# Kernel tuning notes

Measured on AMD Instinct MI355X. Metric: run time of the kernel, lower is better.

## Reference

```python
import jax, jax.numpy as jnp
import numpy as np

B, C, N = 2, 256, 8192
CI = 256  # inter_channels
EPS = 1e-5


def setup_inputs() -> dict:
    key = jax.random.key(0)
    ks = jax.random.split(key, 11)
    s = 1.0 / np.sqrt(C)
    si = 1.0 / np.sqrt(CI)
    return {
        "x": jax.random.normal(ks[0], (B, C, N), dtype=jnp.float32),
        "g_w": jax.random.uniform(ks[1], (CI, C), jnp.float32, -s, s),
        "g_b": jax.random.uniform(ks[2], (CI,), jnp.float32, -s, s),
        "theta_w": jax.random.uniform(ks[3], (CI, C), jnp.float32, -s, s),
        "theta_b": jax.random.uniform(ks[4], (CI,), jnp.float32, -s, s),
        "phi_w": jax.random.uniform(ks[5], (CI, C), jnp.float32, -s, s),
        "phi_b": jax.random.uniform(ks[6], (CI,), jnp.float32, -s, s),
        "w_w": jax.random.uniform(ks[7], (CI, CI), jnp.float32, -si, si),
        "w_b": jax.random.uniform(ks[8], (CI,), jnp.float32, -si, si),
        "bn_gamma": jax.random.normal(ks[9], (CI,), dtype=jnp.float32),
        "bn_beta": jax.random.normal(ks[10], (CI,), dtype=jnp.float32),
    }


def reference(x, g_w, g_b, theta_w, theta_b, phi_w, phi_b, w_w, w_b, bn_gamma, bn_beta):
    # 1x1 Conv1d == channel-wise linear: (o,c) @ (b,c,n) -> (b,o,n)
    g_x = jnp.einsum('oc,bcn->bno', g_w, x) + g_b            # (b, n, ci)
    theta_x = jnp.einsum('oc,bcn->bno', theta_w, x) + theta_b  # (b, n, ci)
    phi_x = jnp.einsum('oc,bcn->bon', phi_w, x) + phi_b[:, None]  # (b, ci, n)
    f = jnp.einsum('bnc,bcm->bnm', theta_x, phi_x)           # (b, n, n), unscaled
    f_div_C = jax.nn.softmax(f, axis=-1)
    y = jnp.einsum('bnm,bmc->bcn', f_div_C, g_x)             # (b, ci, n)
    # W: 1x1 conv then BatchNorm1d (training-mode batch statistics)
    z = jnp.einsum('oc,bcn->bon', w_w, y) + w_b[:, None]     # (b, ci, n)
    mean = jnp.mean(z, axis=(0, 2), keepdims=True)
    var = jnp.mean(jnp.square(z - mean), axis=(0, 2), keepdims=True)  # biased var
    z_hat = (z - mean) * jax.lax.rsqrt(var + EPS)
    out = bn_gamma[:, None] * z_hat + bn_beta[:, None]
    return out
```

## Files before the change

kernel.cpp:

```cpp
#include <hip/hip_runtime.h>
#include <hip/hip_bf16.h>
#include <stdint.h>

#define BB  2
#define CC  256
#define NN  8192
#define CIc 256

typedef __attribute__((ext_vector_type(4)))  float f32x4;
typedef __attribute__((ext_vector_type(16))) float f32x16;
typedef __attribute__((ext_vector_type(8)))  short s16x8;
typedef __attribute__((ext_vector_type(4)))  short s16x4;
typedef __attribute__((ext_vector_type(4)))  int   i32x4;

static __device__ __forceinline__ short f2bf(float f) {
    union { float f; unsigned u; } v; v.f = f;
    unsigned r = (v.u + 0x7FFFu + ((v.u >> 16) & 1u)) >> 16;
    return (short)r;
}
static __device__ __forceinline__ float bf2f(short h) {
    union { unsigned u; float f; } v; v.u = ((unsigned)(unsigned short)h) << 16;
    return v.f;
}

static __device__ __forceinline__ void gload16(const void* g, void* l) {
    __builtin_amdgcn_global_load_lds(
        (const __attribute__((address_space(1))) unsigned int*)g,
        (__attribute__((address_space(3))) unsigned int*)l, 16, 0, 0);
}

__global__ __launch_bounds__(256) void pack_kernel(
    const float* __restrict__ tw, const float* __restrict__ pw,
    const float* __restrict__ gw, const float* __restrict__ ww,
    short* __restrict__ Wf)
{
    int gid  = blockIdx.x * 256 + threadIdx.x;
    int lane = gid & 63;
    int grp  = gid >> 6;
    int ks = grp & 7, ot = (grp >> 3) & 15, m = grp >> 7;
    const float* W = (m == 0) ? tw : (m == 1) ? pw : (m == 2) ? gw : ww;
    const float* p = &W[(size_t)(ot * 16 + (lane & 15)) * 256 + ks * 32 + (lane >> 4) * 8];
    float4 a = *(const float4*)p, c = *(const float4*)(p + 4);
    s16x8 o;
    o[0] = f2bf(a.x); o[1] = f2bf(a.y); o[2] = f2bf(a.z); o[3] = f2bf(a.w);
    o[4] = f2bf(c.x); o[5] = f2bf(c.y); o[6] = f2bf(c.z); o[7] = f2bf(c.w);
    *(s16x8*)&Wf[(size_t)gid * 8] = o;
}

__global__ __launch_bounds__(256) void proj_kernel(
    const float* __restrict__ x, const short* __restrict__ Wf,
    const float* __restrict__ tb, const float* __restrict__ pb,
    const float* __restrict__ gb,
    short* __restrict__ Qb, short* __restrict__ Kf, short* __restrict__ Vf)
{
    __shared__ char xls[64 * 512];
    const int blk = blockIdx.x;
    const int m   = blk % 3;
    const int r2  = blk / 3;
    const int b   = r2 >> 7;
    const int n0  = (r2 & 127) << 6;
    const int tid = threadIdx.x;

    for (int it = 0; it < 16; ++it) {
        int chunk = it * 256 + tid;
        int c  = chunk >> 4;
        int n4 = (chunk & 15) << 2;
        const float4 v = *(const float4*)&x[((size_t)b * CC + c) * NN + n0 + n4];
        float vv[4] = {v.x, v.y, v.z, v.w};
        #pragma unroll
        for (int j = 0; j < 4; ++j) {
            int row = n4 + j;
            int addr = row * 512 + ((c * 2) ^ ((row & 31) << 4));
            *(short*)(xls + addr) = f2bf(vv[j]);
        }
    }
    __syncthreads();

    const int lane = tid & 63, w = tid >> 6;
    const int lo = lane & 15, g = lane >> 4;

    s16x8 bfr[8];
    #pragma unroll
    for (int k = 0; k < 8; ++k) {
        int row = w * 16 + lo;
        int addr = row * 512 + ((k * 64 + g * 16) ^ ((row & 31) << 4));
        bfr[k] = *(const s16x8*)(xls + addr);
    }

    const float* bias = (m == 0) ? tb : (m == 1) ? pb : gb;
    const size_t wfm = (size_t)m * 16 * 8 * 512;

    for (int ot = 0; ot < 16; ++ot) {
        s16x8 afr[8];
        #pragma unroll
        for (int k = 0; k < 8; ++k)
            afr[k] = *(const s16x8*)&Wf[wfm + (size_t)(ot * 8 + k) * 512 + lane * 8];
        f32x4 acc = {0.f, 0.f, 0.f, 0.f};
        if (m < 2) {
            #pragma unroll
            for (int k = 0; k < 8; ++k)
                acc = __builtin_amdgcn_mfma_f32_16x16x32_bf16(afr[k], bfr[k], acc, 0, 0, 0);
        } else {
            #pragma unroll
            for (int k = 0; k < 8; ++k)
                acc = __builtin_amdgcn_mfma_f32_16x16x32_bf16(bfr[k], afr[k], acc, 0, 0, 0);
        }

        if (m == 0) {
            const float4 bi = *(const float4*)&bias[ot * 16 + g * 4];
            int n = n0 + w * 16 + lo;
            s16x4 st;
            st[0] = f2bf(acc[0] + bi.x);
            st[1] = f2bf(acc[1] + bi.y);
            st[2] = f2bf(acc[2] + bi.z);
            st[3] = f2bf(acc[3] + bi.w);
            *(s16x4*)&Qb[((size_t)b * NN + n) * CIc + ot * 16 + g * 4] = st;
        } else if (m == 1) {
            const float4 bi = *(const float4*)&bias[ot * 16 + g * 4];
            int n = n0 + w * 16 + lo;
            s16x4 st;
            st[0] = f2bf(acc[0] + bi.x);
            st[1] = f2bf(acc[1] + bi.y);
            st[2] = f2bf(acc[2] + bi.z);
            st[3] = f2bf(acc[3] + bi.w);
            size_t a = ((((size_t)b * 256 + (n >> 5)) * 16 + ot) * 64
                        + (n & 31) + 32 * (g >> 1)) * 8 + (g & 1) * 4;
            *(s16x4*)&Kf[a] = st;
        } else {
            int nb = n0 + w * 16 + g * 4;
            int o  = ot * 16 + lo;
            float bo = bias[o];
            s16x4 st;
            st[0] = f2bf(acc[0] + bo);
            st[1] = f2bf(acc[1] + bo);
            st[2] = f2bf(acc[2] + bo);
            st[3] = f2bf(acc[3] + bo);
            size_t a = ((((size_t)b * 256 + (nb >> 5)) * 16 + (w & 1) * 8 + (ot >> 1)) * 64
                        + (ot & 1) * 16 + lo + 32 * (g >> 1)) * 8 + (g & 1) * 4;
            *(s16x4*)&Vf[a] = st;
        }
    }
}

template<int SPLIT>
__global__ __launch_bounds__(256, 2) void attn2_kernel(
    const short* __restrict__ Qb, const short* __restrict__ Kf,
    const short* __restrict__ Vf,
    short* __restrict__ part,
    float* __restrict__ ml)
{
    __shared__ char lds[65536];
    const int blk   = blockIdx.x;
    const int combo = blk & (2 * SPLIT - 1);
    const int split = combo >> 1;
    const int b     = combo & 1;
    const int qblk  = blk / (2 * SPLIT);
    const int tid = threadIdx.x, lane = tid & 63, w = tid >> 6;
    const int l31 = lane & 31, h = lane >> 5;
    const int q   = qblk * 128 + w * 32 + l31;
    const size_t bN = (size_t)b * NN;
    const int tgbase = (split * (NN / SPLIT)) >> 5;
    const int NT = (NN / SPLIT) / 32;

    #pragma unroll
    for (int j = 0; j < 8; ++j) {
        const int inst = w * 8 + j;
        if (inst < 16)
            gload16(&Kf[(((size_t)(b * 256 + tgbase) * 16) + inst) * 512 + lane * 8],
                    lds + inst * 1024);
        else
            gload16(&Vf[(((size_t)(b * 256 + tgbase) * 16) + (inst - 16)) * 512 + lane * 8],
                    lds + 16384 + (inst - 16) * 1024);
    }

    s16x8 qf[16];
    #pragma unroll
    for (int ks = 0; ks < 16; ++ks)
        qf[ks] = *(const s16x8*)&Qb[(bN + q) * CIc + ks * 16 + h * 8];

    f32x16 acc[8];
    #pragma unroll
    for (int dt = 0; dt < 8; ++dt)
        #pragma unroll
        for (int r = 0; r < 16; ++r) acc[dt][r] = 0.f;
    float m_use = -1e30f, l_run = 0.f;

    for (int t = 0; t < NT; ++t) {
        __syncthreads();
        const char* cbuf = lds + (t & 1) * 32768;
        const int tg = tgbase + t;
        if (t + 1 < NT) {
            char* nbuf = lds + ((t + 1) & 1) * 32768;
            #pragma unroll
            for (int j = 0; j < 8; ++j) {
                const int inst = w * 8 + j;
                if (inst < 16)
                    gload16(&Kf[(((size_t)(b * 256 + tg + 1) * 16) + inst) * 512 + lane * 8],
                            nbuf + inst * 1024);
                else
                    gload16(&Vf[(((size_t)(b * 256 + tg + 1) * 16) + (inst - 16)) * 512 + lane * 8],
                            nbuf + 16384 + (inst - 16) * 1024);
            }
        }

        f32x16 sacc;
        #pragma unroll
        for (int r = 0; r < 16; ++r) sacc[r] = 0.f;
        __builtin_amdgcn_s_setprio(1);
        #pragma unroll
        for (int ks = 0; ks < 16; ++ks) {
            s16x8 kf = *(const s16x8*)(cbuf + ks * 1024 + lane * 16);
            sacc = __builtin_amdgcn_mfma_f32_32x32x16_bf16(kf, qf[ks], sacc, 0, 0, 0);
        }
        __builtin_amdgcn_s_setprio(0);

        float tmax = fmaxf(sacc[0], sacc[1]);
        #pragma unroll
        for (int r = 2; r < 16; ++r) tmax = fmaxf(tmax, sacc[r]);
        tmax = fmaxf(tmax, __shfl_xor(tmax, 32));
        if (!__all(tmax - m_use <= 8.0f)) {
            float mnew = fmaxf(m_use, tmax);
            float sc = __expf(m_use - mnew);
            l_run *= sc;
            #pragma unroll
            for (int dt = 0; dt < 8; ++dt)
                #pragma unroll
                for (int r = 0; r < 16; ++r) acc[dt][r] *= sc;
            m_use = mnew;
        }
        float sum = 0.f;
        #pragma unroll
        for (int r = 0; r < 16; ++r) {
            float p = __expf(sacc[r] - m_use);
            sacc[r] = p; sum += p;
        }
        sum += __shfl_xor(sum, 32);
        l_run += sum;

        union { int wd[4]; s16x8 v; } f0, f1;
        {
            int w01, w23, w45, w67;
            asm("v_cvt_pk_bf16_f32 %0, %1, %2" : "=v"(w01) : "v"(sacc[0]), "v"(sacc[1]));
            asm("v_cvt_pk_bf16_f32 %0, %1, %2" : "=v"(w23) : "v"(sacc[2]), "v"(sacc[3]));
            asm("v_cvt_pk_bf16_f32 %0, %1, %2" : "=v"(w45) : "v"(sacc[4]), "v"(sacc[5]));
            asm("v_cvt_pk_bf16_f32 %0, %1, %2" : "=v"(w67) : "v"(sacc[6]), "v"(sacc[7]));
            int x01 = __shfl_xor(w01, 32), x23 = __shfl_xor(w23, 32);
            int x45 = __shfl_xor(w45, 32), x67 = __shfl_xor(w67, 32);
            f0.wd[0] = h ? x45 : w01;
            f0.wd[1] = h ? x67 : w23;
            f0.wd[2] = h ? w45 : x01;
            f0.wd[3] = h ? w67 : x23;
        }
        {
            int w01, w23, w45, w67;
            asm("v_cvt_pk_bf16_f32 %0, %1, %2" : "=v"(w01) : "v"(sacc[8]),  "v"(sacc[9]));
            asm("v_cvt_pk_bf16_f32 %0, %1, %2" : "=v"(w23) : "v"(sacc[10]), "v"(sacc[11]));
            asm("v_cvt_pk_bf16_f32 %0, %1, %2" : "=v"(w45) : "v"(sacc[12]), "v"(sacc[13]));
            asm("v_cvt_pk_bf16_f32 %0, %1, %2" : "=v"(w67) : "v"(sacc[14]), "v"(sacc[15]));
            int x01 = __shfl_xor(w01, 32), x23 = __shfl_xor(w23, 32);
            int x45 = __shfl_xor(w45, 32), x67 = __shfl_xor(w67, 32);
            f1.wd[0] = h ? x45 : w01;
            f1.wd[1] = h ? x67 : w23;
            f1.wd[2] = h ? w45 : x01;
            f1.wd[3] = h ? w67 : x23;
        }

        const char* vbuf = cbuf + 16384;
        __builtin_amdgcn_s_setprio(1);
        #pragma unroll
        for (int dt = 0; dt < 8; ++dt) {
            s16x8 v0 = *(const s16x8*)(vbuf + (dt) * 1024 + lane * 16);
            s16x8 v1 = *(const s16x8*)(vbuf + (8 + dt) * 1024 + lane * 16);
            acc[dt] = __builtin_amdgcn_mfma_f32_32x32x16_bf16(v0, f0.v, acc[dt], 0, 0, 0);
            acc[dt] = __builtin_amdgcn_mfma_f32_32x32x16_bf16(v1, f1.v, acc[dt], 0, 0, 0);
        }
        __builtin_amdgcn_s_setprio(0);
    }

    const int qb = qblk * 4 + w;
    const size_t pb2 = (((size_t)(split * 2 + b) * 256 + qb) * 32) * 256;
    #pragma unroll
    for (int dt = 0; dt < 8; ++dt)
        #pragma unroll
        for (int rg = 0; rg < 4; ++rg) {
            s16x4 st;
            st[0] = f2bf(acc[dt][rg * 4 + 0]);
            st[1] = f2bf(acc[dt][rg * 4 + 1]);
            st[2] = f2bf(acc[dt][rg * 4 + 2]);
            st[3] = f2bf(acc[dt][rg * 4 + 3]);
            *(s16x4*)&part[pb2 + (size_t)(dt * 4 + rg) * 256 + lane * 4] = st;
        }
    if (h == 0) {
        size_t mi = ((size_t)split * (BB * NN) + bN + q) * 2;
        ml[mi] = m_use; ml[mi + 1] = l_run;
    }
}

template<int SPLIT>
__global__ __launch_bounds__(256) void combine2_kernel(
    const short* __restrict__ part, const float* __restrict__ ml,
    short* __restrict__ yp)
{
    int gid  = blockIdx.x * 256 + threadIdx.x;
    int lane = gid & 63;
    int slot = (gid >> 6) & 31;
    int qb   = (gid >> 11) & 255;
    int b    = gid >> 19;
    int dt = slot >> 2, rg = slot & 3;
    int l31 = lane & 31, h = lane >> 5;
    int q = qb * 32 + l31;

    float mm[SPLIT], ll[SPLIT];
    float m = -1e30f;
    #pragma unroll
    for (int s = 0; s < SPLIT; ++s) {
        mm[s] = ml[((size_t)s * (BB * NN) + (size_t)b * NN + q) * 2];
        ll[s] = ml[((size_t)s * (BB * NN) + (size_t)b * NN + q) * 2 + 1];
        m = fmaxf(m, mm[s]);
    }
    float den = 0.f, a[SPLIT];
    #pragma unroll
    for (int s = 0; s < SPLIT; ++s) { a[s] = __expf(mm[s] - m); den += a[s] * ll[s]; }
    float o[4] = {0.f, 0.f, 0.f, 0.f};
    #pragma unroll
    for (int s = 0; s < SPLIT; ++s) {
        s16x4 p = *(const s16x4*)&part[((((size_t)(s * 2 + b) * 256 + qb) * 32 + slot) * 64 + lane) * 4];
        #pragma unroll
        for (int j = 0; j < 4; ++j) o[j] += a[s] * bf2f(p[j]);
    }
    float inv = 1.f / den;
    s16x4 st;
    #pragma unroll
    for (int j = 0; j < 4; ++j) st[j] = f2bf(o[j] * inv);
    size_t a2 = ((((size_t)b * 512 + (q >> 4)) * 8 + dt) * 64 + (q & 15) + rg * 16) * 8 + h * 4;
    *(s16x4*)&yp[a2] = st;
}

__global__ __launch_bounds__(256) void zgemm_kernel(
    const short* __restrict__ yp, const short* __restrict__ Wf,
    const float* __restrict__ wb, float* __restrict__ z)
{
    const int blk = blockIdx.x;
    const int b   = blk >> 7;
    const int n0  = (blk & 127) << 6;
    const int tid = threadIdx.x;
    const int lane = tid & 63, w = tid >> 6, lo = lane & 15, g = lane >> 4;

    s16x8 afr[8];
    #pragma unroll
    for (int k = 0; k < 8; ++k)
        afr[k] = *(const s16x8*)&yp[((((size_t)b * 512 + (n0 >> 4) + w) * 8 + k) * 64 + lane) * 8];

    for (int ot = 0; ot < 16; ++ot) {
        f32x4 acc = {0.f, 0.f, 0.f, 0.f};
        #pragma unroll
        for (int k = 0; k < 8; ++k) {
            s16x8 bfr = *(const s16x8*)&Wf[(size_t)((3 * 16 + ot) * 8 + k) * 512 + lane * 8];
            acc = __builtin_amdgcn_mfma_f32_16x16x32_bf16(afr[k], bfr, acc, 0, 0, 0);
        }
        float bias = wb[ot * 16 + lo];
        float4 st = {acc[0] + bias, acc[1] + bias, acc[2] + bias, acc[3] + bias};
        *(float4*)&z[((size_t)b * CIc + ot * 16 + lo) * NN + n0 + w * 16 + g * 4] = st;
    }
}

__global__ __launch_bounds__(256) void bnstats_kernel(
    const float* __restrict__ z, float* __restrict__ stats)
{
    const int o = blockIdx.x;
    const int tid = threadIdx.x;
    float s = 0.f, s2 = 0.f;
    for (int b = 0; b < BB; ++b) {
        const float* row = &z[((size_t)b * CIc + o) * NN];
        for (int i = tid * 4; i < NN; i += 1024) {
            float4 v = *(const float4*)&row[i];
            s  += v.x + v.y + v.z + v.w;
            s2 += v.x * v.x + v.y * v.y + v.z * v.z + v.w * v.w;
        }
    }
    #pragma unroll
    for (int off = 1; off < 64; off <<= 1) {
        s  += __shfl_xor(s, off);
        s2 += __shfl_xor(s2, off);
    }
    __shared__ float rs[8];
    if ((tid & 63) == 0) { rs[tid >> 6] = s; rs[4 + (tid >> 6)] = s2; }
    __syncthreads();
    if (tid == 0) {
        float S  = rs[0] + rs[1] + rs[2] + rs[3];
        float S2 = rs[4] + rs[5] + rs[6] + rs[7];
        float mean = S / (float)(BB * NN);
        float var  = S2 / (float)(BB * NN) - mean * mean;
        stats[o * 2]     = mean;
        stats[o * 2 + 1] = rsqrtf(var + 1e-5f);
    }
}

__global__ __launch_bounds__(256) void bnapply_kernel(
    float* __restrict__ z, const float* __restrict__ stats,
    const float* __restrict__ gamma, const float* __restrict__ beta)
{
    int gid = blockIdx.x * 256 + threadIdx.x;
    int idx4 = gid * 4;
    int o = (idx4 >> 13) & 255;
    float mean = stats[o * 2], rs = stats[o * 2 + 1];
    float ga = gamma[o], be = beta[o];
    float4 v = *(const float4*)&z[idx4];
    v.x = (v.x - mean) * rs * ga + be;
    v.y = (v.y - mean) * rs * ga + be;
    v.z = (v.z - mean) * rs * ga + be;
    v.w = (v.w - mean) * rs * ga + be;
    *(float4*)&z[idx4] = v;
}

extern "C" void kernel_launch(void* const* d_in, const int* in_sizes, int n_in,
                              void* d_out, int out_size, void* d_ws, size_t ws_size,
                              hipStream_t stream) {
    const float* x    = (const float*)d_in[0];
    const float* g_w  = (const float*)d_in[1];
    const float* g_b  = (const float*)d_in[2];
    const float* th_w = (const float*)d_in[3];
    const float* th_b = (const float*)d_in[4];
    const float* ph_w = (const float*)d_in[5];
    const float* ph_b = (const float*)d_in[6];
    const float* w_w  = (const float*)d_in[7];
    const float* w_b  = (const float*)d_in[8];
    const float* bn_g = (const float*)d_in[9];
    const float* bn_b = (const float*)d_in[10];

    char* ws = (char*)d_ws;
    short* Qb    = (short*)ws;
    short* Kf    = (short*)(ws + 8  * 1048576);
    short* Vf    = (short*)(ws + 16 * 1048576);
    float* ml    = (float*)(ws + 24 * 1048576);
    float* stats = (float*)(ws + 24 * 1048576 + 524288);
    short* Wfb   = (short*)(ws + 25 * 1048576);
    float* z     = (float*)d_out;

    const size_t need4 = (size_t)26 * 1048576 + (size_t)4 * BB * NN * CIc * 2;
    const bool  big    = ws_size >= need4;

    pack_kernel<<<128, 256, 0, stream>>>(th_w, ph_w, g_w, w_w, Wfb);
    proj_kernel<<<768, 256, 0, stream>>>(x, Wfb, th_b, ph_b, g_b, Qb, Kf, Vf);

    if (big) {
        short* part = (short*)(ws + 26 * 1048576);
        attn2_kernel<4><<<512, 256, 0, stream>>>(Qb, Kf, Vf, part, ml);
        combine2_kernel<4><<<4096, 256, 0, stream>>>(part, ml, Qb);
    } else {
        short* part = (short*)d_out;
        attn2_kernel<2><<<256, 256, 0, stream>>>(Qb, Kf, Vf, part, ml);
        combine2_kernel<2><<<4096, 256, 0, stream>>>(part, ml, Qb);
    }

    zgemm_kernel<<<256, 256, 0, stream>>>(Qb, Wfb, w_b, z);
    bnstats_kernel<<<256, 256, 0, stream>>>(z, stats);
    bnapply_kernel<<<4096, 256, 0, stream>>>(z, stats, bn_g, bn_b);
}
```

Measured before the change: 222.5 us.

## Fuse split-softmax combine into W GEMM and use permlane32 swap

The split-KV combine step is folded into the W 1x1-conv GEMM kernel. Each block merges the partial attention outputs using the running max and sum values and builds the bf16 A fragments in registers. This removes one kernel launch and the write and read of the intermediate y buffer. The bf16 P-fragment exchange between half-waves now uses permlane32_swap instead of four shuffles plus selects. The fused kernel reads the partials with a different gather pattern that may coalesce less well, and it only runs on the large-workspace path.

```diff
diff --git a/kernel.cpp b/kernel.cpp
--- a/kernel.cpp
+++ b/kernel.cpp
@@ -12,6 +12,7 @@
 typedef __attribute__((ext_vector_type(8)))  short s16x8;
 typedef __attribute__((ext_vector_type(4)))  short s16x4;
 typedef __attribute__((ext_vector_type(4)))  int   i32x4;
+typedef __attribute__((ext_vector_type(2)))  int   i32x2;
 
 static __device__ __forceinline__ short f2bf(float f) {
     union { float f; unsigned u; } v; v.f = f;
@@ -244,12 +245,10 @@
             asm("v_cvt_pk_bf16_f32 %0, %1, %2" : "=v"(w23) : "v"(sacc[2]), "v"(sacc[3]));
             asm("v_cvt_pk_bf16_f32 %0, %1, %2" : "=v"(w45) : "v"(sacc[4]), "v"(sacc[5]));
             asm("v_cvt_pk_bf16_f32 %0, %1, %2" : "=v"(w67) : "v"(sacc[6]), "v"(sacc[7]));
-            int x01 = __shfl_xor(w01, 32), x23 = __shfl_xor(w23, 32);
-            int x45 = __shfl_xor(w45, 32), x67 = __shfl_xor(w67, 32);
-            f0.wd[0] = h ? x45 : w01;
-            f0.wd[1] = h ? x67 : w23;
-            f0.wd[2] = h ? w45 : x01;
-            f0.wd[3] = h ? w67 : x23;
+            i32x2 r02 = __builtin_amdgcn_permlane32_swap(w01, w45, false, false);
+            i32x2 r13 = __builtin_amdgcn_permlane32_swap(w23, w67, false, false);
+            f0.wd[0] = r02[0]; f0.wd[1] = r13[0];
+            f0.wd[2] = r02[1]; f0.wd[3] = r13[1];
         }
         {
             int w01, w23, w45, w67;
@@ -257,12 +256,10 @@
             asm("v_cvt_pk_bf16_f32 %0, %1, %2" : "=v"(w23) : "v"(sacc[10]), "v"(sacc[11]));
             asm("v_cvt_pk_bf16_f32 %0, %1, %2" : "=v"(w45) : "v"(sacc[12]), "v"(sacc[13]));
             asm("v_cvt_pk_bf16_f32 %0, %1, %2" : "=v"(w67) : "v"(sacc[14]), "v"(sacc[15]));
-            int x01 = __shfl_xor(w01, 32), x23 = __shfl_xor(w23, 32);
-            int x45 = __shfl_xor(w45, 32), x67 = __shfl_xor(w67, 32);
-            f1.wd[0] = h ? x45 : w01;
-            f1.wd[1] = h ? x67 : w23;
-            f1.wd[2] = h ? w45 : x01;
-            f1.wd[3] = h ? w67 : x23;
+            i32x2 r02 = __builtin_amdgcn_permlane32_swap(w01, w45, false, false);
+            i32x2 r13 = __builtin_amdgcn_permlane32_swap(w23, w67, false, false);
+            f1.wd[0] = r02[0]; f1.wd[1] = r13[0];
+            f1.wd[2] = r02[1]; f1.wd[3] = r13[1];
         }
 
         const char* vbuf = cbuf + 16384;
@@ -334,6 +331,67 @@
     for (int j = 0; j < 4; ++j) st[j] = f2bf(o[j] * inv);
     size_t a2 = ((((size_t)b * 512 + (q >> 4)) * 8 + dt) * 64 + (q & 15) + rg * 16) * 8 + h * 4;
     *(s16x4*)&yp[a2] = st;
+}
+
+template<int SPLIT>
+__global__ __launch_bounds__(256) void zgemm_fused_kernel(
+    const short* __restrict__ part, const float* __restrict__ ml,
+    const short* __restrict__ Wf, const float* __restrict__ wb,
+    float* __restrict__ z)
+{
+    const int blk = blockIdx.x;
+    const int b   = blk >> 7;
+    const int n0  = (blk & 127) << 6;
+    const int tid = threadIdx.x;
+    const int lane = tid & 63, w = tid >> 6, lo = lane & 15, g = lane >> 4;
+    const int q  = n0 + w * 16 + lo;
+    const int qb = q >> 5, l31 = q & 31;
+
+    float mm[SPLIT], ll[SPLIT], a[SPLIT];
+    float m = -1e30f;
+    #pragma unroll
+    for (int s = 0; s < SPLIT; ++s) {
+        mm[s] = ml[((size_t)s * (BB * NN) + (size_t)b * NN + q) * 2];
+        ll[s] = ml[((size_t)s * (BB * NN) + (size_t)b * NN + q) * 2 + 1];
+        m = fmaxf(m, mm[s]);
+    }
+    float den = 0.f;
+    #pragma unroll
+    for (int s = 0; s < SPLIT; ++s) { a[s] = __expf(mm[s] - m); den += a[s] * ll[s]; }
+    float inv = 1.f / den;
+    #pragma unroll
+    for (int s = 0; s < SPLIT; ++s) a[s] *= inv;
+
+    s16x8 afr[8];
+    #pragma unroll
+    for (int k = 0; k < 8; ++k) {
+        float o[8] = {0.f, 0.f, 0.f, 0.f, 0.f, 0.f, 0.f, 0.f};
+        #pragma unroll
+        for (int s = 0; s < SPLIT; ++s) {
+            size_t base = ((((size_t)(s * 2 + b) * 256 + qb) * 32 + (k * 4 + g)) * 64 + l31) * 4;
+            s16x4 plo = *(const s16x4*)&part[base];
+            s16x4 phi = *(const s16x4*)&part[base + 128];
+            #pragma unroll
+            for (int j = 0; j < 4; ++j) {
+                o[j]     += a[s] * bf2f(plo[j]);
+                o[4 + j] += a[s] * bf2f(phi[j]);
+            }
+        }
+        #pragma unroll
+        for (int j = 0; j < 8; ++j) afr[k][j] = f2bf(o[j]);
+    }
+
+    for (int ot = 0; ot < 16; ++ot) {
+        f32x4 acc = {0.f, 0.f, 0.f, 0.f};
+        #pragma unroll
+        for (int k = 0; k < 8; ++k) {
+            s16x8 bfr = *(const s16x8*)&Wf[(size_t)((3 * 16 + ot) * 8 + k) * 512 + lane * 8];
+            acc = __builtin_amdgcn_mfma_f32_16x16x32_bf16(afr[k], bfr, acc, 0, 0, 0);
+        }
+        float bias = wb[ot * 16 + lo];
+        float4 st = {acc[0] + bias, acc[1] + bias, acc[2] + bias, acc[3] + bias};
+        *(float4*)&z[((size_t)b * CIc + ot * 16 + lo) * NN + n0 + w * 16 + g * 4] = st;
+    }
 }
 
 __global__ __launch_bounds__(256) void zgemm_kernel(
@@ -446,14 +504,14 @@
     if (big) {
         short* part = (short*)(ws + 26 * 1048576);
         attn2_kernel<4><<<512, 256, 0, stream>>>(Qb, Kf, Vf, part, ml);
-        combine2_kernel<4><<<4096, 256, 0, stream>>>(part, ml, Qb);
+        zgemm_fused_kernel<4><<<256, 256, 0, stream>>>(part, ml, Wfb, w_b, z);
     } else {
         short* part = (short*)d_out;
         attn2_kernel<2><<<256, 256, 0, stream>>>(Qb, Kf, Vf, part, ml);
         combine2_kernel<2><<<4096, 256, 0, stream>>>(part, ml, Qb);
-    }
-
-    zgemm_kernel<<<256, 256, 0, stream>>>(Qb, Wfb, w_b, z);
+        zgemm_kernel<<<256, 256, 0, stream>>>(Qb, Wfb, w_b, z);
+    }
+
     bnstats_kernel<<<256, 256, 0, stream>>>(z, stats);
     bnapply_kernel<<<4096, 256, 0, stream>>>(z, stats, bn_g, bn_b);
 }
```

Result: faster. 213.6 us (-4.0%).
